# Performance work log

Measured on AMD Instinct MI355X. Metric: run time of the kernel, lower is better.

## Reference

```python
import jax, jax.numpy as jnp
import numpy as np

# Model constants (match init_kwargs + mamba_ssm defaults)
CIN, COUT, K, STRIDE = 64, 128, 4, 4
D = 128            # d_model = features_out
DI = 256           # d_inner = 2*D (expand=2)
NSTATE = 16        # d_state
DCONV = 4          # depthwise conv width
DT_RANK = 8        # ceil(D/16)
NB = 3             # blocks per direction
NTOT = 2 * NB      # forward + backward stacks


def setup_inputs() -> dict:
    key = jax.random.key(0)
    ks = jax.random.split(key, 10)
    s = 0.02
    x = jax.random.normal(ks[0], (2, CIN, 8192), jnp.float32)
    convd_w = jax.random.normal(ks[1], (COUT, CIN, K), jnp.float32) * s
    convd_b = jnp.zeros((COUT,), jnp.float32)
    ln_w = jnp.ones((NTOT, D), jnp.float32)
    ln_b = jnp.zeros((NTOT, D), jnp.float32)
    in_proj_w = jax.random.normal(ks[2], (NTOT, 2 * DI, D), jnp.float32) * s
    conv_w = jax.random.normal(ks[3], (NTOT, DI, DCONV), jnp.float32) * s
    conv_b = jnp.zeros((NTOT, DI), jnp.float32)
    xproj_w = jax.random.normal(ks[4], (NTOT, DT_RANK + 2 * NSTATE, DI), jnp.float32) * s
    dtproj_w = jax.random.normal(ks[5], (NTOT, DI, DT_RANK), jnp.float32) * s
    dtproj_b = jax.random.normal(ks[6], (NTOT, DI), jnp.float32) * s
    # S4D-real init: A = -[1..N]
    A_log = jnp.log(jnp.broadcast_to(jnp.arange(1, NSTATE + 1, dtype=jnp.float32), (NTOT, DI, NSTATE)))
    Dparam = jnp.ones((NTOT, DI), jnp.float32)
    outproj_w = jax.random.normal(ks[7], (NTOT, D, DI), jnp.float32) * s
    return dict(x=x, convd_w=convd_w, convd_b=convd_b, ln_w=ln_w, ln_b=ln_b,
                in_proj_w=in_proj_w, conv_w=conv_w, conv_b=conv_b, xproj_w=xproj_w,
                dtproj_w=dtproj_w, dtproj_b=dtproj_b, A_log=A_log, Dparam=Dparam,
                outproj_w=outproj_w)


def _silu(x):
    return x * jax.nn.sigmoid(x)


def _layernorm(x, w, b, eps=1e-5):
    m = x.mean(-1, keepdims=True)
    xc = x - m
    v = (xc * xc).mean(-1, keepdims=True)
    return xc * jax.lax.rsqrt(v + eps) * w + b


def _mamba_mixer(x, in_proj_w, conv_w, conv_b, xproj_w, dtproj_w, dtproj_b, A_log, Dp, outproj_w):
    # x: (B, L, D)
    B, L, _ = x.shape
    xz = jnp.einsum('bld,ed->ble', x, in_proj_w)          # (B, L, 2*DI)
    xm, z = jnp.split(xz, 2, axis=-1)
    # causal depthwise conv (pad left DCONV-1, truncate to L)
    xp = jnp.pad(xm, ((0, 0), (DCONV - 1, 0), (0, 0)))
    xc = conv_b
    acc = jnp.zeros_like(xm)
    for k in range(DCONV):
        acc = acc + xp[:, k:k + L, :] * conv_w[:, k]
    xc = _silu(acc + conv_b)                               # (B, L, DI)
    dbc = jnp.einsum('ble,ne->bln', xc, xproj_w)           # (B, L, DT_RANK + 2N)
    dt, Bc, Cc = jnp.split(dbc, [DT_RANK, DT_RANK + NSTATE], axis=-1)
    dt = jax.nn.softplus(jnp.einsum('blr,dr->bld', dt, dtproj_w) + dtproj_b)  # (B, L, DI)
    A = -jnp.exp(A_log)                                    # (DI, N)
    dA = jnp.exp(dt[..., None] * A)                        # (B, L, DI, N)
    dBx = dt[..., None] * Bc[:, :, None, :] * xc[..., None]

    def step(h, inp):
        dA_t, dBx_t, C_t = inp
        h = dA_t * h + dBx_t                               # (B, DI, N)
        y = jnp.einsum('bdn,bn->bd', h, C_t)
        return h, y

    h0 = jnp.zeros((B, DI, NSTATE), x.dtype)
    _, ys = jax.lax.scan(step, h0, (jnp.swapaxes(dA, 0, 1), jnp.swapaxes(dBx, 0, 1), jnp.swapaxes(Cc, 0, 1)))
    y = jnp.swapaxes(ys, 0, 1)                             # (B, L, DI)
    y = (y + Dp * xc) * _silu(z)
    return jnp.einsum('ble,de->bld', y, outproj_w)         # (B, L, D)


def _mamba_stack(x, off, ln_w, ln_b, in_proj_w, conv_w, conv_b, xproj_w, dtproj_w, dtproj_b, A_log, Dparam, outproj_w):
    # mamba_ssm Block semantics: residual = x (+ prev residual); x = mixer(norm(residual))
    res = None
    cur = x
    for i in range(NB):
        j = off + i
        res = cur if res is None else cur + res
        hn = _layernorm(res, ln_w[j], ln_b[j])
        cur = _mamba_mixer(hn, in_proj_w[j], conv_w[j], conv_b[j], xproj_w[j],
                           dtproj_w[j], dtproj_b[j], A_log[j], Dparam[j], outproj_w[j])
    return cur, res


def reference(x, convd_w, convd_b, ln_w, ln_b, in_proj_w, conv_w, conv_b, xproj_w,
              dtproj_w, dtproj_b, A_log, Dparam, outproj_w):
    # downsampling conv + SiLU
    y = jax.lax.conv_general_dilated(x, convd_w, (STRIDE,), 'VALID',
                                     dimension_numbers=('NCH', 'OIH', 'NCH'))
    y = _silu(y + convd_b[None, :, None])                  # (B, COUT, L')
    h = jnp.swapaxes(y, 1, 2)                              # (B, L', D)
    xf, rf = _mamba_stack(h, 0, ln_w, ln_b, in_proj_w, conv_w, conv_b, xproj_w,
                          dtproj_w, dtproj_b, A_log, Dparam, outproj_w)
    xb, rb = _mamba_stack(h[:, ::-1, :], NB, ln_w, ln_b, in_proj_w, conv_w, conv_b, xproj_w,
                          dtproj_w, dtproj_b, A_log, Dparam, outproj_w)
    out = (xf + rf) + (xb + rb)[:, ::-1, :]
    return jnp.swapaxes(out, 1, 2), rf, rb
```

## Files before the change

### kernel.cpp

```cpp
#include <hip/hip_runtime.h>
#include <hip/hip_bf16.h>
#include <math.h>

#define B    2
#define CIN  64
#define LIN  8192
#define L    2048
#define D    128
#define DI   256
#define NS   16
#define RK   8
#define NSTREAM 4
#define CH   32
#define NCH  (L/CH)
#define TOK  (NSTREAM*L)
#define SZ_D ((size_t)TOK*D)
#define SZ_DI ((size_t)TOK*DI)
#define SXM 280
#define SHN 152

typedef short  bfrag __attribute__((ext_vector_type(8)));
typedef float  facc  __attribute__((ext_vector_type(4)));
#define MFMA __builtin_amdgcn_mfma_f32_16x16x32_bf16

__device__ __forceinline__ float sigmoidf_(float x){ return 1.f/(1.f+__expf(-x)); }
__device__ __forceinline__ float siluf_(float x){ return x*sigmoidf_(x); }
__device__ __forceinline__ ushort f2bf(float f){
    unsigned u = __float_as_uint(f);
    u += 0x7fffu + ((u>>16)&1u);
    return (ushort)(u>>16);
}
__device__ __forceinline__ float bf2f(ushort u){ return __uint_as_float(((unsigned)u)<<16); }
__device__ __forceinline__ float softplusf_(float t){
    return (t > 20.f) ? t : __logf(1.f + __expf(t));
}

__global__ void k_cvtall(const float* __restrict__ cw, const float* __restrict__ ipw,
                         const float* __restrict__ opw, const float* __restrict__ xpw,
                         ushort* __restrict__ dst){
    int i = blockIdx.x*256 + threadIdx.x;
    ushort v;
    if (i < 32768)       v = f2bf(cw[i]);
    else if (i < 425984) v = f2bf(ipw[i-32768]);
    else if (i < 622592) v = f2bf(opw[i-425984]);
    else {
        int t = i - 622592;
        int k = t & 255, nr = (t>>8) & 63, j = t>>14;
        v = (nr < 40) ? f2bf(xpw[((size_t)j*40 + nr)*256 + k]) : (ushort)0;
    }
    dst[i] = v;
}

__global__ void k_down(const float* __restrict__ x, const ushort* __restrict__ wd,
                       const float* __restrict__ bias, float* __restrict__ h){
    __shared__ ushort sxd[64*SXM];
    int tid = threadIdx.x;
    int m0 = blockIdx.x*64;
    int b = m0 >> 11;
    int l0 = m0 & 2047;
    for (int idx = tid; idx < 64*64; idx += 256){
        int t = idx & 63, cc = idx >> 6;
        float4 v = *(const float4*)(x + ((size_t)(b*CIN + cc))*LIN + 4*(l0+t));
        ushort4 o; o.x=f2bf(v.x); o.y=f2bf(v.y); o.z=f2bf(v.z); o.w=f2bf(v.w);
        *(ushort4*)&sxd[t*SXM + cc*4] = o;
    }
    __syncthreads();
    int w = tid>>6, lane = tid&63, rw = w>>1, cw = w&1;
    int q = lane>>4, r = lane&15;
    int n0 = blockIdx.y*64 + cw*32;
    const ushort* b0p = wd + (size_t)(n0 + r)*256 + q*8;
    const ushort* b1p = b0p + (size_t)16*256;
    facc acc[2][2] = {};
    #pragma unroll
    for (int kb=0; kb<8; ++kb){
        bfrag a0 = *(bfrag*)&sxd[(rw*32 + r)*SXM + kb*32 + q*8];
        bfrag a1 = *(bfrag*)&sxd[(rw*32 + 16 + r)*SXM + kb*32 + q*8];
        bfrag b0 = *(const bfrag*)(b0p + kb*32);
        bfrag b1 = *(const bfrag*)(b1p + kb*32);
        acc[0][0] = MFMA(a0,b0,acc[0][0],0,0,0);
        acc[0][1] = MFMA(a0,b1,acc[0][1],0,0,0);
        acc[1][0] = MFMA(a1,b0,acc[1][0],0,0,0);
        acc[1][1] = MFMA(a1,b1,acc[1][1],0,0,0);
    }
    #pragma unroll
    for (int im=0; im<2; ++im)
    #pragma unroll
    for (int in=0; in<2; ++in){
        int col = n0 + in*16 + r;
        float bv = bias[col];
        #pragma unroll
        for (int r2=0; r2<4; ++r2){
            int row = m0 + rw*32 + im*16 + q*4 + r2;
            int bb = row >> 11, l = row & 2047;
            float v = siluf_(acc[im][in][r2] + bv);
            h[((size_t)(bb*L + l))*D + col] = v;
            h[((size_t)((2+bb)*L + (L-1-l)))*D + col] = v;
        }
    }
}

__global__ void __launch_bounds__(256,1)
k_head(const float* __restrict__ curIn, const float* __restrict__ resIn,
       float* __restrict__ resOut,
       const float* __restrict__ lnw, const float* __restrict__ lnb,
       const ushort* __restrict__ wbi, const ushort* __restrict__ wbx,
       const float* __restrict__ cw, const float* __restrict__ cb,
       const float* __restrict__ Wdt, const float* __restrict__ bdt,
       const float* __restrict__ A_log,
       ushort* __restrict__ zb, ushort* __restrict__ xcb,
       float* __restrict__ dtr, float* __restrict__ Bc, float* __restrict__ Cc,
       float* __restrict__ Aprod, float* __restrict__ Bend, int blk, int first){
    __shared__ ushort smHn[35*SHN];
    __shared__ ushort smXm[35*SXM];
    __shared__ float  smDbc[32*68];
    const int tid = threadIdx.x;
    const int bi = blockIdx.x;
    const int s = bi >> 6, c = bi & 63;
    const int j = (s>>1)*3 + blk;
    const int base_tok = s*L + c*CH;

    {
        int t = tid >> 3, g8 = tid & 7;
        size_t off = (size_t)(base_tok + t)*D + g8*16;
        float4 v[4];
        const float4* cp = (const float4*)(curIn + off);
        #pragma unroll
        for (int i=0;i<4;++i) v[i] = cp[i];
        if (!first){
            const float4* rp = (const float4*)(resIn + off);
            #pragma unroll
            for (int i=0;i<4;++i){ float4 rv=rp[i]; v[i].x+=rv.x; v[i].y+=rv.y; v[i].z+=rv.z; v[i].w+=rv.w; }
        }
        {
            float4* ro = (float4*)(resOut + off);
            #pragma unroll
            for (int i=0;i<4;++i) ro[i] = v[i];
        }
        float s1=0.f, s2=0.f;
        #pragma unroll
        for (int i=0;i<4;++i){
            s1 += v[i].x+v[i].y+v[i].z+v[i].w;
            s2 += v[i].x*v[i].x+v[i].y*v[i].y+v[i].z*v[i].z+v[i].w*v[i].w;
        }
        s1 += __shfl_xor(s1,1); s2 += __shfl_xor(s2,1);
        s1 += __shfl_xor(s1,2); s2 += __shfl_xor(s2,2);
        s1 += __shfl_xor(s1,4); s2 += __shfl_xor(s2,4);
        float mean = s1*(1.f/128.f);
        float var  = s2*(1.f/128.f) - mean*mean;
        float rstd = rsqrtf(var + 1e-5f);
        const float4* lwp = (const float4*)(lnw + j*D + g8*16);
        const float4* lbp = (const float4*)(lnb + j*D + g8*16);
        #pragma unroll
        for (int i=0;i<4;++i){
            float4 lw = lwp[i], lb = lbp[i];
            ushort4 o;
            o.x = f2bf((v[i].x-mean)*rstd*lw.x + lb.x);
            o.y = f2bf((v[i].y-mean)*rstd*lw.y + lb.y);
            o.z = f2bf((v[i].z-mean)*rstd*lw.z + lb.z);
            o.w = f2bf((v[i].w-mean)*rstd*lw.w + lb.w);
            *(ushort4*)&smHn[t*SHN + g8*16 + i*4] = o;
        }
    }
    if (c > 0 && tid < 24){
        int t = tid >> 3, g8 = tid & 7;
        size_t off = (size_t)(base_tok - 3 + t)*D + g8*16;
        float4 v[4];
        const float4* cp = (const float4*)(curIn + off);
        #pragma unroll
        for (int i=0;i<4;++i) v[i] = cp[i];
        if (!first){
            const float4* rp = (const float4*)(resIn + off);
            #pragma unroll
            for (int i=0;i<4;++i){ float4 rv=rp[i]; v[i].x+=rv.x; v[i].y+=rv.y; v[i].z+=rv.z; v[i].w+=rv.w; }
        }
        float s1=0.f, s2=0.f;
        #pragma unroll
        for (int i=0;i<4;++i){
            s1 += v[i].x+v[i].y+v[i].z+v[i].w;
            s2 += v[i].x*v[i].x+v[i].y*v[i].y+v[i].z*v[i].z+v[i].w*v[i].w;
        }
        s1 += __shfl_xor(s1,1); s2 += __shfl_xor(s2,1);
        s1 += __shfl_xor(s1,2); s2 += __shfl_xor(s2,2);
        s1 += __shfl_xor(s1,4); s2 += __shfl_xor(s2,4);
        float mean = s1*(1.f/128.f);
        float var  = s2*(1.f/128.f) - mean*mean;
        float rstd = rsqrtf(var + 1e-5f);
        const float4* lwp = (const float4*)(lnw + j*D + g8*16);
        const float4* lbp = (const float4*)(lnb + j*D + g8*16);
        #pragma unroll
        for (int i=0;i<4;++i){
            float4 lw = lwp[i], lb = lbp[i];
            ushort4 o;
            o.x = f2bf((v[i].x-mean)*rstd*lw.x + lb.x);
            o.y = f2bf((v[i].y-mean)*rstd*lw.y + lb.y);
            o.z = f2bf((v[i].z-mean)*rstd*lw.z + lb.z);
            o.w = f2bf((v[i].w-mean)*rstd*lw.w + lb.w);
            *(ushort4*)&smHn[(32+t)*SHN + g8*16 + i*4] = o;
        }
    }
    __syncthreads();

    {
        int w = tid>>6, lane = tid&63, q = lane>>4, r = lane&15;
        bfrag a[3][4];
        #pragma unroll
        for (int rt=0; rt<3; ++rt)
        #pragma unroll
        for (int kb=0; kb<4; ++kb)
            a[rt][kb] = *(bfrag*)&smHn[(rt*16 + r)*SHN + kb*32 + q*8];
        #pragma unroll
        for (int ct=0; ct<8; ++ct){
            int n0 = w*128 + ct*16;
            const ushort* bp = wbi + ((size_t)j*512 + n0 + r)*128 + q*8;
            facc a0 = {}, a1 = {}, a2 = {};
            #pragma unroll
            for (int kb=0; kb<4; ++kb){
                bfrag bv = *(const bfrag*)(bp + kb*32);
                a0 = MFMA(a[0][kb], bv, a0, 0,0,0);
                a1 = MFMA(a[1][kb], bv, a1, 0,0,0);
                a2 = MFMA(a[2][kb], bv, a2, 0,0,0);
            }
            int colL = n0 + r;
            if (colL < DI){
                #pragma unroll
                for (int r2=0;r2<4;++r2){
                    int rr = q*4 + r2;
                    smXm[rr*SXM + colL]      = f2bf(a0[r2]);
                    smXm[(16+rr)*SXM + colL] = f2bf(a1[r2]);
                    if (rr < 3) smXm[(32+rr)*SXM + colL] = f2bf(a2[r2]);
                }
            } else {
                int cz = colL - DI;
                #pragma unroll
                for (int r2=0;r2<4;++r2){
                    int rr = q*4 + r2;
                    zb[(size_t)(base_tok + rr)*DI + cz]      = f2bf(a0[r2]);
                    zb[(size_t)(base_tok + 16 + rr)*DI + cz] = f2bf(a1[r2]);
                }
            }
        }
    }
    __syncthreads();

    {
        const float* w4 = cw + ((size_t)j*DI + tid)*4;
        float cw0=w4[0], cw1=w4[1], cw2=w4[2], cw3=w4[3];
        float cbb = cb[j*DI + tid];
        float xm1=0.f, xm2=0.f, xm3=0.f;
        if (c > 0){
            xm3 = bf2f(smXm[32*SXM + tid]);
            xm2 = bf2f(smXm[33*SXM + tid]);
            xm1 = bf2f(smXm[34*SXM + tid]);
        }
        #pragma unroll 4
        for (int i=0;i<CH;++i){
            float x0 = bf2f(smXm[i*SXM + tid]);
            float v = siluf_(cbb + cw3*x0 + cw2*xm1 + cw1*xm2 + cw0*xm3);
            ushort us = f2bf(v);
            smXm[i*SXM + tid] = us;
            xcb[(size_t)(base_tok+i)*DI + tid] = us;
            xm3 = xm2; xm2 = xm1; xm1 = x0;
        }
    }
    __syncthreads();

    {
        int w = tid>>6, lane = tid&63, q = lane>>4, r = lane&15;
        facc a0 = {}, a1 = {};
        const ushort* bp = wbx + ((size_t)j*64 + w*16 + r)*256 + q*8;
        #pragma unroll
        for (int kb=0; kb<8; ++kb){
            bfrag av0 = *(bfrag*)&smXm[r*SXM + kb*32 + q*8];
            bfrag av1 = *(bfrag*)&smXm[(16+r)*SXM + kb*32 + q*8];
            bfrag bv  = *(const bfrag*)(bp + kb*32);
            a0 = MFMA(av0, bv, a0, 0,0,0);
            a1 = MFMA(av1, bv, a1, 0,0,0);
        }
        int col = w*16 + r;
        #pragma unroll
        for (int r2=0;r2<4;++r2){
            int rr = q*4 + r2;
            smDbc[rr*68 + col]      = a0[r2];
            smDbc[(16+rr)*68 + col] = a1[r2];
            int row0 = base_tok + rr, row1 = base_tok + 16 + rr;
            if      (col < 8){  dtr[(size_t)row0*RK + col] = a0[r2];      dtr[(size_t)row1*RK + col] = a1[r2]; }
            else if (col < 24){ Bc [(size_t)row0*NS + (col-8)] = a0[r2];  Bc [(size_t)row1*NS + (col-8)] = a1[r2]; }
            else if (col < 40){ Cc [(size_t)row0*NS + (col-24)] = a0[r2]; Cc [(size_t)row1*NS + (col-24)] = a1[r2]; }
        }
    }
    __syncthreads();

    {
        float A[NS], wv[RK];
        const float* ar = A_log + ((size_t)j*DI + tid)*NS;
        #pragma unroll
        for (int n=0;n<NS;++n) A[n] = -__expf(ar[n]);
        const float* wr = Wdt + ((size_t)j*DI + tid)*RK;
        #pragma unroll
        for (int r=0;r<RK;++r) wv[r] = wr[r];
        float bb2 = bdt[j*DI + tid];
        float ap[NS], hs[NS];
        #pragma unroll
        for (int n=0;n<NS;++n){ ap[n]=1.f; hs[n]=0.f; }
        #pragma unroll 4
        for (int l=0;l<CH;++l){
            float t = bb2;
            #pragma unroll
            for (int r=0;r<RK;++r) t += smDbc[l*68+r]*wv[r];
            float dtv = softplusf_(t);
            float xv  = bf2f(smXm[l*SXM + tid]);
            float dbx = dtv*xv;
            #pragma unroll
            for (int n=0;n<NS;++n){
                float dA = __expf(dtv*A[n]);
                ap[n] *= dA;
                hs[n] = dA*hs[n] + dbx*smDbc[l*68+8+n];
            }
        }
        size_t pb = (size_t)bi*4096 + tid;
        #pragma unroll
        for (int n=0;n<NS;++n){
            Aprod[pb + (size_t)n*256] = ap[n];
            Bend [pb + (size_t)n*256] = hs[n];
        }
    }
}

__global__ void k_scanmid(const float* __restrict__ Aprod, float* __restrict__ Bend){
    int tid = blockIdx.x*128 + threadIdx.x;
    int s = tid >> 12;
    int nd = tid & 4095;
    size_t base = (size_t)s*NCH*4096 + nd;
    float h = 0.f;
    for (int c0=0; c0<NCH; c0+=16){
        float a[16], b[16];
        #pragma unroll
        for (int i=0;i<16;++i){
            a[i] = Aprod[base + (size_t)(c0+i)*4096];
            b[i] = Bend [base + (size_t)(c0+i)*4096];
        }
        #pragma unroll
        for (int i=0;i<16;++i){
            Bend[base + (size_t)(c0+i)*4096] = h;
            h = a[i]*h + b[i];
        }
    }
}

__global__ void k_tail(const float* __restrict__ dtr, const ushort* __restrict__ xcb,
                       const float* __restrict__ Bc, const float* __restrict__ Cc,
                       const float* __restrict__ A_log,
                       const float* __restrict__ Wdt, const float* __restrict__ bdt,
                       const float* __restrict__ h0, const ushort* __restrict__ zb,
                       const float* __restrict__ Dp, const ushort* __restrict__ wbo,
                       float* __restrict__ cur, int blk){
    int c = blockIdx.x, s = blockIdx.y; int j = (s>>1)*3 + blk;
    int d = threadIdx.x;
    __shared__ float sB[CH*NS], sC[CH*NS], sdtr[CH*RK];
    __shared__ ushort sg[CH*SXM];
    int base_tok = s*L + c*CH;
    sB[d]     = Bc[(size_t)base_tok*NS + d];
    sB[256+d] = Bc[(size_t)base_tok*NS + 256 + d];
    sC[d]     = Cc[(size_t)base_tok*NS + d];
    sC[256+d] = Cc[(size_t)base_tok*NS + 256 + d];
    sdtr[d]   = dtr[(size_t)base_tok*RK + d];
    float A[NS], wv[RK];
    const float* ar = A_log + ((size_t)j*DI + d)*NS;
    #pragma unroll
    for (int n=0;n<NS;++n) A[n] = -__expf(ar[n]);
    const float* wr = Wdt + ((size_t)j*DI + d)*RK;
    #pragma unroll
    for (int r=0;r<RK;++r) wv[r] = wr[r];
    float bb = bdt[j*DI + d];
    float Dpd = Dp[j*DI + d];
    float hs[NS];
    size_t pb = (size_t)(s*NCH + c)*4096 + d;
    #pragma unroll
    for (int n=0;n<NS;++n) hs[n] = h0[pb + (size_t)n*256];
    __syncthreads();
    #pragma unroll 4
    for (int l=0;l<CH;++l){
        float t = bb;
        #pragma unroll
        for (int r=0;r<RK;++r) t += sdtr[l*RK+r]*wv[r];
        float dtv = softplusf_(t);
        float xv  = bf2f(xcb[(size_t)(base_tok+l)*DI + d]);
        float dbx = dtv*xv;
        float p = 0.f;
        #pragma unroll
        for (int n=0;n<NS;++n){
            float dA = __expf(dtv*A[n]);
            hs[n] = dA*hs[n] + dbx*sB[l*NS+n];
            p += hs[n]*sC[l*NS+n];
        }
        float zv = bf2f(zb[(size_t)(base_tok+l)*DI + d]);
        sg[l*SXM + d] = f2bf((p + Dpd*xv)*siluf_(zv));
    }
    __syncthreads();
    int w = d>>6, lane = d&63, q = lane>>4, r = lane&15;
    facc acc[2][2] = {};
    const ushort* b0p = wbo + ((size_t)j*128 + w*32 + r)*256 + q*8;
    const ushort* b1p = b0p + 16*256;
    #pragma unroll
    for (int kb=0; kb<8; ++kb){
        bfrag av0 = *(bfrag*)&sg[r*SXM + kb*32 + q*8];
        bfrag av1 = *(bfrag*)&sg[(16+r)*SXM + kb*32 + q*8];
        bfrag bv0 = *(const bfrag*)(b0p + kb*32);
        bfrag bv1 = *(const bfrag*)(b1p + kb*32);
        acc[0][0] = MFMA(av0,bv0,acc[0][0],0,0,0);
        acc[0][1] = MFMA(av0,bv1,acc[0][1],0,0,0);
        acc[1][0] = MFMA(av1,bv0,acc[1][0],0,0,0);
        acc[1][1] = MFMA(av1,bv1,acc[1][1],0,0,0);
    }
    #pragma unroll
    for (int rt=0; rt<2; ++rt)
    #pragma unroll
    for (int ct=0; ct<2; ++ct){
        int col = w*32 + ct*16 + r;
        #pragma unroll
        for (int r2=0;r2<4;++r2){
            int row = base_tok + rt*16 + q*4 + r2;
            cur[(size_t)row*D + col] = acc[rt][ct][r2];
        }
    }
}

__global__ void k_final(const float* __restrict__ cur, const float* __restrict__ res,
                        float* __restrict__ out){
    __shared__ float tile[128*33];
    int tid = threadIdx.x;
    int c = blockIdx.x, b = blockIdx.y;
    int t = tid>>3, g8 = tid&7;
    int lf = c*32 + t, lb = L-1-lf;
    size_t fo = ((size_t)(b*L + lf))*D + g8*16;
    size_t bo = ((size_t)((2+b)*L + lb))*D + g8*16;
    #pragma unroll
    for (int i=0;i<4;++i){
        float4 cf  = *(const float4*)(cur + fo + i*4);
        float4 rf  = *(const float4*)(res + fo + i*4);
        float4 cb2 = *(const float4*)(cur + bo + i*4);
        float4 rb2 = *(const float4*)(res + bo + i*4);
        int db = g8*16 + i*4;
        tile[(db+0)*33 + t] = cf.x+rf.x+cb2.x+rb2.x;
        tile[(db+1)*33 + t] = cf.y+rf.y+cb2.y+rb2.y;
        tile[(db+2)*33 + t] = cf.z+rf.z+cb2.z+rb2.z;
        tile[(db+3)*33 + t] = cf.w+rf.w+cb2.w+rb2.w;
    }
    __syncthreads();
    int d = tid>>1, hf = tid&1;
    size_t obase = ((size_t)(b*D + d))*L + c*32 + hf*16;
    #pragma unroll
    for (int i=0;i<4;++i){
        float4 o4;
        o4.x = tile[d*33 + hf*16 + i*4 + 0];
        o4.y = tile[d*33 + hf*16 + i*4 + 1];
        o4.z = tile[d*33 + hf*16 + i*4 + 2];
        o4.w = tile[d*33 + hf*16 + i*4 + 3];
        *(float4*)(out + obase + i*4) = o4;
    }
    const float4* src = (const float4*)res;
    float4* dst = (float4*)(out + (size_t)2*D*L);
    for (int idx = (blockIdx.y*NCH + blockIdx.x)*256 + tid; idx < 262144; idx += 2*NCH*256)
        dst[idx] = src[idx];
}

extern "C" void kernel_launch(void* const* d_in, const int* in_sizes, int n_in,
                              void* d_out, int out_size, void* d_ws, size_t ws_size,
                              hipStream_t stream){
    const float* x         = (const float*)d_in[0];
    const float* convd_w   = (const float*)d_in[1];
    const float* convd_b   = (const float*)d_in[2];
    const float* ln_w      = (const float*)d_in[3];
    const float* ln_b      = (const float*)d_in[4];
    const float* in_proj_w = (const float*)d_in[5];
    const float* conv_w    = (const float*)d_in[6];
    const float* conv_b    = (const float*)d_in[7];
    const float* xproj_w   = (const float*)d_in[8];
    const float* dtproj_w  = (const float*)d_in[9];
    const float* dtproj_b  = (const float*)d_in[10];
    const float* A_log     = (const float*)d_in[11];
    const float* Dparam    = (const float*)d_in[12];
    const float* outproj_w = (const float*)d_in[13];

    float* ws = (float*)d_ws;
    float* h     = ws; ws += SZ_D;
    float* res0  = ws; ws += SZ_D;
    float* res1  = ws; ws += SZ_D;
    float* cur   = ws; ws += SZ_D;
    float* Aprod = ws; ws += SZ_D;
    float* Bend  = ws; ws += SZ_D;
    float* dtr   = ws; ws += (size_t)TOK*RK;
    float* Bc    = ws; ws += (size_t)TOK*NS;
    float* Cc    = ws; ws += (size_t)TOK*NS;
    ushort* zb   = (ushort*)ws; ws += SZ_DI/2;
    ushort* xcb  = (ushort*)ws; ws += SZ_DI/2;
    ushort* wall = (ushort*)ws;
    ushort* wbd  = wall;
    ushort* wbi  = wall + 32768;
    ushort* wbo  = wall + 425984;
    ushort* wbx  = wall + 622592;

    k_cvtall<<<2816, 256, 0, stream>>>(convd_w, in_proj_w, outproj_w, xproj_w, wall);
    k_down<<<dim3(64, 2), 256, 0, stream>>>(x, wbd, convd_b, h);

    float* resin[3]  = { nullptr, res0, res1 };
    float* resout[3] = { res0,    res1, res0 };
    for (int blk = 0; blk < 3; ++blk){
        const float* ci = (blk==0) ? h : cur;
        const float* ri = (blk==0) ? h : resin[blk];
        k_head<<<NSTREAM*NCH, 256, 0, stream>>>(ci, ri, resout[blk], ln_w, ln_b, wbi, wbx,
                                                conv_w, conv_b, dtproj_w, dtproj_b, A_log,
                                                zb, xcb, dtr, Bc, Cc, Aprod, Bend, blk, blk==0);
        k_scanmid<<<128, 128, 0, stream>>>(Aprod, Bend);
        k_tail<<<dim3(NCH, NSTREAM), 256, 0, stream>>>(dtr, xcb, Bc, Cc, A_log,
                                                       dtproj_w, dtproj_b, Bend, zb,
                                                       Dparam, wbo, cur, blk);
    }

    k_final<<<dim3(NCH, B), 256, 0, stream>>>(cur, res0, (float*)d_out);
}
```

Baseline: 258.6 us.

## Fold chunk-prefix scan into tail kernel and write residual directly to output

Removes the separate chunk-carry scan kernel: each tail block now recomputes its starting SSM state by serially combining the per-chunk (Aprod, Bend) pairs of all earlier chunks, using a per-thread float4 layout with a prefetch of the next chunk. The residual buffer res0 is aliased onto the output region, so the final kernel no longer copies it. k_head's launch bounds are relaxed to allow two blocks per CU. In exchange, later chunks do redundant O(c) serial work with global loads, up to 63 steps, which creates load imbalance across tail blocks.

```diff
diff --git a/kernel.cpp b/kernel.cpp
--- a/kernel.cpp
+++ b/kernel.cpp
@@ -99,7 +99,7 @@
     }
 }
 
-__global__ void __launch_bounds__(256,1)
+__global__ void __launch_bounds__(256,2)
 k_head(const float* __restrict__ curIn, const float* __restrict__ resIn,
        float* __restrict__ resOut,
        const float* __restrict__ lnw, const float* __restrict__ lnb,
@@ -317,32 +317,12 @@
                 hs[n] = dA*hs[n] + dbx*smDbc[l*68+8+n];
             }
         }
-        size_t pb = (size_t)bi*4096 + tid;
-        #pragma unroll
-        for (int n=0;n<NS;++n){
-            Aprod[pb + (size_t)n*256] = ap[n];
-            Bend [pb + (size_t)n*256] = hs[n];
-        }
-    }
-}
-
-__global__ void k_scanmid(const float* __restrict__ Aprod, float* __restrict__ Bend){
-    int tid = blockIdx.x*128 + threadIdx.x;
-    int s = tid >> 12;
-    int nd = tid & 4095;
-    size_t base = (size_t)s*NCH*4096 + nd;
-    float h = 0.f;
-    for (int c0=0; c0<NCH; c0+=16){
-        float a[16], b[16];
-        #pragma unroll
-        for (int i=0;i<16;++i){
-            a[i] = Aprod[base + (size_t)(c0+i)*4096];
-            b[i] = Bend [base + (size_t)(c0+i)*4096];
-        }
-        #pragma unroll
-        for (int i=0;i<16;++i){
-            Bend[base + (size_t)(c0+i)*4096] = h;
-            h = a[i]*h + b[i];
+        float4* Ap4 = (float4*)(Aprod + (size_t)bi*4096 + tid*16);
+        float4* Bp4 = (float4*)(Bend  + (size_t)bi*4096 + tid*16);
+        #pragma unroll
+        for (int nq=0;nq<4;++nq){
+            Ap4[nq] = *(float4*)&ap[nq*4];
+            Bp4[nq] = *(float4*)&hs[nq*4];
         }
     }
 }
@@ -351,7 +331,8 @@
                        const float* __restrict__ Bc, const float* __restrict__ Cc,
                        const float* __restrict__ A_log,
                        const float* __restrict__ Wdt, const float* __restrict__ bdt,
-                       const float* __restrict__ h0, const ushort* __restrict__ zb,
+                       const float* __restrict__ Aprod, const float* __restrict__ Bend,
+                       const ushort* __restrict__ zb,
                        const float* __restrict__ Dp, const ushort* __restrict__ wbo,
                        float* __restrict__ cur, int blk){
     int c = blockIdx.x, s = blockIdx.y; int j = (s>>1)*3 + blk;
@@ -373,10 +354,39 @@
     for (int r=0;r<RK;++r) wv[r] = wr[r];
     float bb = bdt[j*DI + d];
     float Dpd = Dp[j*DI + d];
+
     float hs[NS];
-    size_t pb = (size_t)(s*NCH + c)*4096 + d;
-    #pragma unroll
-    for (int n=0;n<NS;++n) hs[n] = h0[pb + (size_t)n*256];
+    #pragma unroll
+    for (int n=0;n<NS;++n) hs[n] = 0.f;
+    {
+        size_t sbase = (size_t)(s*NCH)*4096 + d*16;
+        float4 a4[4], b4[4], a4n[4], b4n[4];
+        if (c > 0){
+            const float4* A4 = (const float4*)(Aprod + sbase);
+            const float4* B4 = (const float4*)(Bend  + sbase);
+            #pragma unroll
+            for (int nq=0;nq<4;++nq){ a4[nq]=A4[nq]; b4[nq]=B4[nq]; }
+        }
+        for (int k=0; k<c; ++k){
+            if (k+1 < c){
+                const float4* A4 = (const float4*)(Aprod + sbase + (size_t)(k+1)*4096);
+                const float4* B4 = (const float4*)(Bend  + sbase + (size_t)(k+1)*4096);
+                #pragma unroll
+                for (int nq=0;nq<4;++nq){ a4n[nq]=A4[nq]; b4n[nq]=B4[nq]; }
+            }
+            #pragma unroll
+            for (int nq=0;nq<4;++nq){
+                float4 h4 = *(float4*)&hs[nq*4];
+                h4.x = a4[nq].x*h4.x + b4[nq].x;
+                h4.y = a4[nq].y*h4.y + b4[nq].y;
+                h4.z = a4[nq].z*h4.z + b4[nq].z;
+                h4.w = a4[nq].w*h4.w + b4[nq].w;
+                *(float4*)&hs[nq*4] = h4;
+            }
+            #pragma unroll
+            for (int nq=0;nq<4;++nq){ a4[nq]=a4n[nq]; b4[nq]=b4n[nq]; }
+        }
+    }
     __syncthreads();
     #pragma unroll 4
     for (int l=0;l<CH;++l){
@@ -458,10 +468,6 @@
         o4.w = tile[d*33 + hf*16 + i*4 + 3];
         *(float4*)(out + obase + i*4) = o4;
     }
-    const float4* src = (const float4*)res;
-    float4* dst = (float4*)(out + (size_t)2*D*L);
-    for (int idx = (blockIdx.y*NCH + blockIdx.x)*256 + tid; idx < 262144; idx += 2*NCH*256)
-        dst[idx] = src[idx];
 }
 
 extern "C" void kernel_launch(void* const* d_in, const int* in_sizes, int n_in,
@@ -482,9 +488,10 @@
     const float* Dparam    = (const float*)d_in[12];
     const float* outproj_w = (const float*)d_in[13];
 
+    float* res0 = (float*)d_out + (size_t)2*D*L;
+
     float* ws = (float*)d_ws;
     float* h     = ws; ws += SZ_D;
-    float* res0  = ws; ws += SZ_D;
     float* res1  = ws; ws += SZ_D;
     float* cur   = ws; ws += SZ_D;
     float* Aprod = ws; ws += SZ_D;
@@ -511,9 +518,8 @@
         k_head<<<NSTREAM*NCH, 256, 0, stream>>>(ci, ri, resout[blk], ln_w, ln_b, wbi, wbx,
                                                 conv_w, conv_b, dtproj_w, dtproj_b, A_log,
                                                 zb, xcb, dtr, Bc, Cc, Aprod, Bend, blk, blk==0);
-        k_scanmid<<<128, 128, 0, stream>>>(Aprod, Bend);
         k_tail<<<dim3(NCH, NSTREAM), 256, 0, stream>>>(dtr, xcb, Bc, Cc, A_log,
-                                                       dtproj_w, dtproj_b, Bend, zb,
+                                                       dtproj_w, dtproj_b, Aprod, Bend, zb,
                                                        Dparam, wbo, cur, blk);
     }
 
```

After: 326.5 us. +26.2%, slower.
